# Kernel optimization log

Hardware: AMD Instinct MI355X
Metric: run time of the kernel (lower is better)

## Reference

```python
import jax, jax.numpy as jnp
import numpy as np

H = 512   # hidden_size
V = 128   # vec_size / output_size
L = 8192  # sequence length


def _gru_cell(x, h, Wih, Whh, bih, bhh):
    # torch GRU cell: gates ordered (r, z, n)
    gx = x @ Wih.T + bih            # [3H]
    gh = h @ Whh.T + bhh            # [3H]
    xr, xz, xn = jnp.split(gx, 3)
    hr, hz, hn = jnp.split(gh, 3)
    r = jax.nn.sigmoid(xr + hr)
    z = jax.nn.sigmoid(xz + hz)
    n = jnp.tanh(xn + r * hn)
    return (1.0 - z) * n + z * h


def _run_gru2(xs, h0, h1, p0, p1):
    """2-layer GRU over xs [L, in]; returns ((h0_f, h1_f), top-layer outputs [L, H])."""
    def step(carry, x):
        c0, c1 = carry
        c0 = _gru_cell(x, c0, *p0)
        c1 = _gru_cell(c0, c1, *p1)
        return (c0, c1), c1
    return jax.lax.scan(step, (h0, h1), xs)


def setup_inputs() -> dict:
    key = jax.random.key(0)
    ks = jax.random.split(key, 24)
    b = 1.0 / np.sqrt(H)  # torch default uniform init bound
    u = lambda k, shape: jax.random.uniform(k, shape, jnp.float32, -b, b)
    inp = {
        "src": jax.random.normal(ks[0], (L, V), jnp.float32),
        "trg": jax.random.uniform(ks[1], (L, V), jnp.float32),
        # encoder GRU (input V -> hidden H, 2 layers)
        "enc_Wih0": u(ks[2], (3 * H, V)),  "enc_Whh0": u(ks[3], (3 * H, H)),
        "enc_bih0": u(ks[4], (3 * H,)),    "enc_bhh0": u(ks[5], (3 * H,)),
        "enc_Wih1": u(ks[6], (3 * H, H)),  "enc_Whh1": u(ks[7], (3 * H, H)),
        "enc_bih1": u(ks[8], (3 * H,)),    "enc_bhh1": u(ks[9], (3 * H,)),
        # decoder GRU (input V -> hidden H, 2 layers)
        "dec_Wih0": u(ks[10], (3 * H, V)), "dec_Whh0": u(ks[11], (3 * H, H)),
        "dec_bih0": u(ks[12], (3 * H,)),   "dec_bhh0": u(ks[13], (3 * H,)),
        "dec_Wih1": u(ks[14], (3 * H, H)), "dec_Whh1": u(ks[15], (3 * H, H)),
        "dec_bih1": u(ks[16], (3 * H,)),   "dec_bhh1": u(ks[17], (3 * H,)),
        # output projection
        "Wout": u(ks[18], (V, H)), "bout": u(ks[19], (V,)),
    }
    return inp


def reference(src, trg,
              enc_Wih0, enc_Whh0, enc_bih0, enc_bhh0,
              enc_Wih1, enc_Whh1, enc_bih1, enc_bhh1,
              dec_Wih0, dec_Whh0, dec_bih0, dec_bhh0,
              dec_Wih1, dec_Whh1, dec_bih1, dec_bhh1,
              Wout, bout):
    z = jnp.zeros((H,), src.dtype)
    # Encoder: run 2-layer GRU over src, keep final per-layer states
    (h0, h1), _ = _run_gru2(
        src, z, z,
        (enc_Wih0, enc_Whh0, enc_bih0, enc_bhh0),
        (enc_Wih1, enc_Whh1, enc_bih1, enc_bhh1))
    # Decoder inputs under full teacher forcing: trg[0], trg[0], trg[1], ... trg[L-2]
    dec_in = jax.nn.relu(jnp.concatenate([trg[:1], trg[:-1]], axis=0))  # [L, V]
    _, ys = _run_gru2(
        dec_in, h0, h1,
        (dec_Wih0, dec_Whh0, dec_bih0, dec_bhh0),
        (dec_Wih1, dec_Whh1, dec_bih1, dec_bhh1))  # ys: [L, H] top-layer outputs
    outputs = jax.nn.sigmoid(ys @ Wout.T + bout)   # [L, V]
    return outputs
```

## Files before the change

### kernel.cpp

```cpp
#include <hip/hip_runtime.h>

#define Hh   512
#define Vv   128
#define LL   8192
#define G3   1536
#define NBK  256
#define S0   16
#define S1   4

#define RECBYTES ((S0*512 + S1*512) * 8ull)
#define OFF_GX   0ull
#define OFF_YS   50331648ull
#define OFF_RECE 67108864ull
#define OFF_RECD (OFF_RECE + RECBYTES)
#define OFF_WT   (OFF_RECD + RECBYTES)

#define H1OFF (S0*512)

__device__ __forceinline__ float sigm(float x)  { return 1.f / (1.f + __expf(-x)); }
__device__ __forceinline__ float tanha(float x) { return 2.f / (1.f + __expf(-2.f * x)) - 1.f; }

__device__ __forceinline__ unsigned long long packpair(float v, int t) {
    return ((unsigned long long)(unsigned)t << 32) | (unsigned long long)__float_as_uint(v);
}
__device__ __forceinline__ int   pair_tag(unsigned long long p) { return (int)(p >> 32); }
__device__ __forceinline__ float pair_val(unsigned long long p) { return __uint_as_float((unsigned)p); }

template <int CTRL>
__device__ __forceinline__ float dpp_add(float m) {
    int t = __builtin_amdgcn_update_dpp(0, __builtin_bit_cast(int, m), CTRL, 0xF, 0xF, true);
    return m + __builtin_bit_cast(float, t);
}
__device__ __forceinline__ float red2(float a, float c, int lane) {
    a = dpp_add<0xB1>(a);
    c = dpp_add<0xB1>(c);
    float m = (lane & 1) ? c : a;
    m = dpp_add<0x122>(m);
    m = dpp_add<0x124>(m);
    m = dpp_add<0x128>(m);
    m += __shfl_xor(m, 16);
    m += __shfl_xor(m, 32);
    return m;
}

__global__ __launch_bounds__(256) void gemm_gx(
    const float* __restrict__ X, const float* __restrict__ Wih,
    const float* __restrict__ bih, float* __restrict__ gxo, int shift_relu)
{
    __shared__ float xs[16][128];
    const int tid = threadIdx.x;
    const int m0  = blockIdx.x * 16;
    const int c   = blockIdx.y * 256 + tid;

    for (int i = tid; i < 16 * 128; i += 256) {
        const int r = i >> 7, k = i & 127;
        int srow = m0 + r;
        if (shift_relu) srow = (srow == 0) ? 0 : (srow - 1);
        float v = X[(size_t)srow * Vv + k];
        if (shift_relu) v = fmaxf(v, 0.f);
        xs[r][k] = v;
    }
    __syncthreads();

    const float4* wp = (const float4*)(Wih + (size_t)c * Vv);
    float4 wr[32];
#pragma unroll
    for (int q = 0; q < 32; ++q) wr[q] = wp[q];
    const float bb = bih[c];

    for (int m = 0; m < 16; ++m) {
        const float4* xp = (const float4*)xs[m];
        float acc = bb;
#pragma unroll
        for (int q = 0; q < 32; ++q) {
            const float4 x4 = xp[q];
            acc = fmaf(wr[q].x, x4.x, acc); acc = fmaf(wr[q].y, x4.y, acc);
            acc = fmaf(wr[q].z, x4.z, acc); acc = fmaf(wr[q].w, x4.w, acc);
        }
        gxo[(size_t)(m0 + m) * G3 + c] = acc;
    }
}

__global__ __launch_bounds__(64, 1) void seq2(
    const float* __restrict__ gx,
    const float* __restrict__ Whh0, const float* __restrict__ Wih1,
    const float* __restrict__ Whh1,
    const float* __restrict__ bhh0, const float* __restrict__ bih1,
    const float* __restrict__ bhh1,
    unsigned long long* __restrict__ rec,
    float* __restrict__ ys)
{
    const int bid = blockIdx.x, lane = threadIdx.x;
    unsigned long long* h0rec = rec;
    unsigned long long* h1rec = rec + H1OFF;

    if (bid < 128) {
        const int e0 = 4 * bid;
        int off[8];
#pragma unroll
        for (int j = 0; j < 8; ++j) off[j] = (e0 + lane + 64 * j) & 511;

        float w[12][8];
#pragma unroll
        for (int g = 0; g < 3; ++g)
#pragma unroll
            for (int i = 0; i < 4; ++i) {
                const float* row = Whh0 + (size_t)(g * Hh + e0 + i) * Hh;
#pragma unroll
                for (int j = 0; j < 8; ++j) w[g * 4 + i][j] = row[off[j]];
            }

        float b_r = 0.f, b_z = 0.f, b_n = 0.f;
        if (lane < 4) {
            const int e = e0 + lane;
            b_r = bhh0[e]; b_z = bhh0[Hh + e]; b_n = bhh0[2 * Hh + e];
        }
        float xr = 0.f, xz = 0.f, xn = 0.f;
        if (lane < 4) {
            xr = gx[e0 + lane]; xz = gx[Hh + e0 + lane]; xn = gx[2 * Hh + e0 + lane];
        }

        for (int t = 0; t < LL; ++t) {
            const int need = t - 1;
            const unsigned long long* rp = h0rec + (size_t)((t + S0 - 1) & (S0 - 1)) * 512;
            unsigned long long p[8];
            int ok;
            do {
#pragma unroll
                for (int j = 0; j < 8; ++j)
                    p[j] = __hip_atomic_load(rp + off[j], __ATOMIC_RELAXED, __HIP_MEMORY_SCOPE_AGENT);
                ok = 1;
#pragma unroll
                for (int j = 0; j < 8; ++j) ok &= (pair_tag(p[j]) >= need);
            } while (!__all(ok));

            if ((t & 7) == 0) {
                const int gneed = t - 4;
                const unsigned long long* gp = h1rec + (size_t)(t & (S1 - 1)) * 512;
                int gok;
                do {
                    gok = 1;
#pragma unroll
                    for (int j = 0; j < 8; ++j) {
                        const unsigned long long q = __hip_atomic_load(
                            gp + ((lane + 64 * j) & 511), __ATOMIC_RELAXED, __HIP_MEMORY_SCOPE_AGENT);
                        gok &= (pair_tag(q) >= gneed);
                    }
                } while (!__all(gok));
            }

            float nxr = 0.f, nxz = 0.f, nxn = 0.f;
            if (lane < 4 && t + 1 < LL) {
                const size_t gb = (size_t)(t + 1) * G3 + e0 + lane;
                nxr = gx[gb]; nxz = gx[gb + Hh]; nxn = gx[gb + 2 * Hh];
            }

            float h0v[8];
#pragma unroll
            for (int j = 0; j < 8; ++j) h0v[j] = pair_val(p[j]);

            float acc[12];
#pragma unroll
            for (int r = 0; r < 12; ++r) acc[r] = 0.f;
#pragma unroll
            for (int j = 0; j < 8; ++j)
#pragma unroll
                for (int r = 0; r < 12; ++r) acc[r] = fmaf(w[r][j], h0v[j], acc[r]);

            float sred[6];
#pragma unroll
            for (int k = 0; k < 6; ++k) sred[k] = red2(acc[2 * k], acc[2 * k + 1], lane);

            if (lane < 4) {
                const int i2 = lane >> 1;
                const float rg = sigm(xr + sred[i2] + b_r);
                const float zg = sigm(xz + sred[2 + i2] + b_z);
                const float ng = tanha(xn + rg * (sred[4 + i2] + b_n));
                const float hnew = (1.f - zg) * ng + zg * h0v[0];
                __hip_atomic_store(h0rec + (size_t)(t & (S0 - 1)) * 512 + e0 + lane,
                                   packpair(hnew, t), __ATOMIC_RELAXED, __HIP_MEMORY_SCOPE_AGENT);
            }
            xr = nxr; xz = nxz; xn = nxn;
        }
    } else {
        const int e0 = 4 * (bid - 128);
        int off[8];
#pragma unroll
        for (int j = 0; j < 8; ++j) off[j] = (e0 + lane + 64 * j) & 511;

        float wA[12][8], wB[12][8];
#pragma unroll
        for (int g = 0; g < 3; ++g)
#pragma unroll
            for (int i = 0; i < 4; ++i) {
                const float* rowA = Wih1 + (size_t)(g * Hh + e0 + i) * Hh;
                const float* rowB = Whh1 + (size_t)(g * Hh + e0 + i) * Hh;
#pragma unroll
                for (int j = 0; j < 8; ++j) {
                    wA[g * 4 + i][j] = rowA[off[j]];
                    wB[g * 4 + i][j] = rowB[off[j]];
                }
            }

        float b_r = 0.f, b_z = 0.f, b_n1 = 0.f, b_n2 = 0.f;
        if (lane < 4) {
            const int e = e0 + lane;
            b_r  = bih1[e] + bhh1[e];
            b_z  = bih1[Hh + e] + bhh1[Hh + e];
            b_n1 = bih1[2 * Hh + e];
            b_n2 = bhh1[2 * Hh + e];
        }

        for (int t = 0; t < LL; ++t) {
            const unsigned long long* rp0 = h0rec + (size_t)(t & (S0 - 1)) * 512;
            const unsigned long long* rp1 = h1rec + (size_t)((t + S1 - 1) & (S1 - 1)) * 512;
            unsigned long long p0[8], p1[8];
            int ok;
            do {
#pragma unroll
                for (int j = 0; j < 8; ++j)
                    p0[j] = __hip_atomic_load(rp0 + off[j], __ATOMIC_RELAXED, __HIP_MEMORY_SCOPE_AGENT);
#pragma unroll
                for (int j = 0; j < 8; ++j)
                    p1[j] = __hip_atomic_load(rp1 + off[j], __ATOMIC_RELAXED, __HIP_MEMORY_SCOPE_AGENT);
                ok = 1;
#pragma unroll
                for (int j = 0; j < 8; ++j)
                    ok &= (pair_tag(p0[j]) >= t) & (pair_tag(p1[j]) >= t - 1);
            } while (!__all(ok));

            float h0v[8], h1v[8];
#pragma unroll
            for (int j = 0; j < 8; ++j) { h0v[j] = pair_val(p0[j]); h1v[j] = pair_val(p1[j]); }

            float acc[16];
#pragma unroll
            for (int r = 0; r < 16; ++r) acc[r] = 0.f;
#pragma unroll
            for (int j = 0; j < 8; ++j) {
#pragma unroll
                for (int r = 0; r < 8; ++r) {
                    acc[r] = fmaf(wA[r][j], h0v[j], acc[r]);
                    acc[r] = fmaf(wB[r][j], h1v[j], acc[r]);
                }
#pragma unroll
                for (int i = 0; i < 4; ++i) {
                    acc[8 + i]  = fmaf(wA[8 + i][j], h0v[j], acc[8 + i]);
                    acc[12 + i] = fmaf(wB[8 + i][j], h1v[j], acc[12 + i]);
                }
            }

            float sred[8];
#pragma unroll
            for (int k = 0; k < 8; ++k) sred[k] = red2(acc[2 * k], acc[2 * k + 1], lane);

            if (lane < 4) {
                const int i2 = lane >> 1;
                const float rg = sigm(sred[i2] + b_r);
                const float zg = sigm(sred[2 + i2] + b_z);
                const float ng = tanha(sred[4 + i2] + b_n1 + rg * (sred[6 + i2] + b_n2));
                const float hnew = (1.f - zg) * ng + zg * h1v[0];
                if (ys) ys[(size_t)t * Hh + e0 + lane] = hnew;
                __hip_atomic_store(h1rec + (size_t)(t & (S1 - 1)) * 512 + e0 + lane,
                                   packpair(hnew, t), __ATOMIC_RELAXED, __HIP_MEMORY_SCOPE_AGENT);
            }
        }
    }
}

__global__ __launch_bounds__(256) void transposeW(const float* __restrict__ W,
                                                  float* __restrict__ WT,
                                                  unsigned long long* __restrict__ encr)
{
    const int i = blockIdx.x * 256 + threadIdx.x;
    WT[(i & 511) * 128 + (i >> 9)] = W[i];
    if (i < S0 * 512) {
        const int slot = i >> 9;
        __hip_atomic_store(encr + i, packpair(0.f, (slot == S0 - 1) ? -1 : -100),
                           __ATOMIC_RELAXED, __HIP_MEMORY_SCOPE_AGENT);
    }
    if (i < S1 * 512) {
        const int slot = i >> 9;
        __hip_atomic_store(encr + H1OFF + i, packpair(0.f, (slot == S1 - 1) ? -1 : slot - 4),
                           __ATOMIC_RELAXED, __HIP_MEMORY_SCOPE_AGENT);
    }
}

__global__ __launch_bounds__(256) void handoff(const unsigned long long* __restrict__ encr,
                                               unsigned long long* __restrict__ decr)
{
    const int p = blockIdx.x * 256 + threadIdx.x;
    {
        const int slot = p >> 9;
        unsigned long long v;
        if (slot == S0 - 1) {
            const unsigned long long src = __hip_atomic_load(
                encr + p, __ATOMIC_RELAXED, __HIP_MEMORY_SCOPE_AGENT);
            v = packpair(pair_val(src), -1);
        } else {
            v = packpair(0.f, -100);
        }
        __hip_atomic_store(decr + p, v, __ATOMIC_RELAXED, __HIP_MEMORY_SCOPE_AGENT);
    }
    if (p < S1 * 512) {
        const int slot = p >> 9;
        unsigned long long v;
        if (slot == S1 - 1) {
            const unsigned long long src = __hip_atomic_load(
                encr + H1OFF + p, __ATOMIC_RELAXED, __HIP_MEMORY_SCOPE_AGENT);
            v = packpair(pair_val(src), -1);
        } else {
            v = packpair(0.f, slot - 4);
        }
        __hip_atomic_store(decr + H1OFF + p, v, __ATOMIC_RELAXED, __HIP_MEMORY_SCOPE_AGENT);
    }
}

__global__ __launch_bounds__(128) void out_proj(
    const float* __restrict__ ys, const float* __restrict__ WT,
    const float* __restrict__ bout, float* __restrict__ out)
{
    __shared__ float yss[16][512];
    const int tid = threadIdx.x;
    const int m0  = blockIdx.x * 16;

    for (int i = tid; i < 16 * 512; i += 128)
        yss[i >> 9][i & 511] = ys[(size_t)(m0 + (i >> 9)) * 512 + (i & 511)];
    __syncthreads();

    const int c = tid;
    float acc[16];
    const float b = bout[c];
#pragma unroll
    for (int m = 0; m < 16; ++m) acc[m] = b;

    for (int k4 = 0; k4 < 128; ++k4) {
        const float w0 = WT[(4 * k4 + 0) * 128 + c];
        const float w1 = WT[(4 * k4 + 1) * 128 + c];
        const float w2 = WT[(4 * k4 + 2) * 128 + c];
        const float w3 = WT[(4 * k4 + 3) * 128 + c];
#pragma unroll
        for (int m = 0; m < 16; ++m) {
            const float4 yv = *(const float4*)&yss[m][4 * k4];
            acc[m] = fmaf(w0, yv.x, fmaf(w1, yv.y, fmaf(w2, yv.z, fmaf(w3, yv.w, acc[m]))));
        }
    }
#pragma unroll
    for (int m = 0; m < 16; ++m)
        out[(size_t)(m0 + m) * 128 + c] = 1.f / (1.f + __expf(-acc[m]));
}

extern "C" void kernel_launch(void* const* d_in, const int* in_sizes, int n_in,
                              void* d_out, int out_size, void* d_ws, size_t ws_size,
                              hipStream_t stream)
{
    const float* src      = (const float*)d_in[0];
    const float* trg      = (const float*)d_in[1];
    const float* eWih0    = (const float*)d_in[2];
    const float* eWhh0    = (const float*)d_in[3];
    const float* ebih0    = (const float*)d_in[4];
    const float* ebhh0    = (const float*)d_in[5];
    const float* eWih1    = (const float*)d_in[6];
    const float* eWhh1    = (const float*)d_in[7];
    const float* ebih1    = (const float*)d_in[8];
    const float* ebhh1    = (const float*)d_in[9];
    const float* dWih0    = (const float*)d_in[10];
    const float* dWhh0    = (const float*)d_in[11];
    const float* dbih0    = (const float*)d_in[12];
    const float* dbhh0    = (const float*)d_in[13];
    const float* dWih1    = (const float*)d_in[14];
    const float* dWhh1    = (const float*)d_in[15];
    const float* dbih1    = (const float*)d_in[16];
    const float* dbhh1    = (const float*)d_in[17];
    const float* Wout     = (const float*)d_in[18];
    const float* bout     = (const float*)d_in[19];

    char* ws = (char*)d_ws;
    float*              gx   = (float*)(ws + OFF_GX);
    float*              ys   = (float*)(ws + OFF_YS);
    unsigned long long* recE = (unsigned long long*)(ws + OFF_RECE);
    unsigned long long* recD = (unsigned long long*)(ws + OFF_RECD);
    float*              WT   = (float*)(ws + OFF_WT);

    hipLaunchKernelGGL(transposeW, dim3(256), dim3(256), 0, stream, Wout, WT, recE);

    hipLaunchKernelGGL(gemm_gx, dim3(LL / 16, 6), dim3(256), 0, stream,
                       src, eWih0, ebih0, gx, 0);
    hipLaunchKernelGGL(seq2, dim3(NBK), dim3(64), 0, stream,
                       gx, eWhh0, eWih1, eWhh1, ebhh0, ebih1, ebhh1,
                       recE, (float*)nullptr);

    hipLaunchKernelGGL(handoff, dim3(32), dim3(256), 0, stream, recE, recD);
    hipLaunchKernelGGL(gemm_gx, dim3(LL / 16, 6), dim3(256), 0, stream,
                       trg, dWih0, dbih0, gx, 1);
    hipLaunchKernelGGL(seq2, dim3(NBK), dim3(64), 0, stream,
                       gx, dWhh0, dWih1, dWhh1, dbhh0, dbih1, dbhh1,
                       recD, ys);

    hipLaunchKernelGGL(out_proj, dim3(LL / 16), dim3(128), 0, stream,
                       ys, WT, bout, (float*)d_out);

    (void)in_sizes; (void)n_in; (void)out_size; (void)ws_size;
}
```

Measured before the change: 32.26 ms.

## Consume hidden-state chunks incrementally while spinning and deepen layer-0 ring buffer

```diff
diff --git a/kernel.cpp b/kernel.cpp
--- a/kernel.cpp
+++ b/kernel.cpp
@@ -5,7 +5,7 @@
 #define LL   8192
 #define G3   1536
 #define NBK  256
-#define S0   16
+#define S0   64
 #define S1   4
 
 #define RECBYTES ((S0*512 + S1*512) * 8ull)
@@ -123,19 +123,30 @@
         for (int t = 0; t < LL; ++t) {
             const int need = t - 1;
             const unsigned long long* rp = h0rec + (size_t)((t + S0 - 1) & (S0 - 1)) * 512;
-            unsigned long long p[8];
-            int ok;
+            float acc[12];
+#pragma unroll
+            for (int r = 0; r < 12; ++r) acc[r] = 0.f;
+            float h0self = 0.f;
+            unsigned done = 0;
             do {
+                unsigned long long p[8];
 #pragma unroll
                 for (int j = 0; j < 8; ++j)
                     p[j] = __hip_atomic_load(rp + off[j], __ATOMIC_RELAXED, __HIP_MEMORY_SCOPE_AGENT);
-                ok = 1;
-#pragma unroll
-                for (int j = 0; j < 8; ++j) ok &= (pair_tag(p[j]) >= need);
-            } while (!__all(ok));
-
-            if ((t & 7) == 0) {
-                const int gneed = t - 4;
+#pragma unroll
+                for (int j = 0; j < 8; ++j) {
+                    if (done == (unsigned)j && pair_tag(p[j]) >= need) {
+                        const float v = pair_val(p[j]);
+                        if (j == 0) h0self = v;
+#pragma unroll
+                        for (int r = 0; r < 12; ++r) acc[r] = fmaf(w[r][j], v, acc[r]);
+                        done = j + 1;
+                    }
+                }
+            } while (!__all(done == 8u));
+
+            if ((t & 31) == 0) {
+                const int gneed = t - 16;
                 const unsigned long long* gp = h1rec + (size_t)(t & (S1 - 1)) * 512;
                 int gok;
                 do {
@@ -155,18 +166,6 @@
                 nxr = gx[gb]; nxz = gx[gb + Hh]; nxn = gx[gb + 2 * Hh];
             }
 
-            float h0v[8];
-#pragma unroll
-            for (int j = 0; j < 8; ++j) h0v[j] = pair_val(p[j]);
-
-            float acc[12];
-#pragma unroll
-            for (int r = 0; r < 12; ++r) acc[r] = 0.f;
-#pragma unroll
-            for (int j = 0; j < 8; ++j)
-#pragma unroll
-                for (int r = 0; r < 12; ++r) acc[r] = fmaf(w[r][j], h0v[j], acc[r]);
-
             float sred[6];
 #pragma unroll
             for (int k = 0; k < 6; ++k) sred[k] = red2(acc[2 * k], acc[2 * k + 1], lane);
@@ -176,7 +175,7 @@
                 const float rg = sigm(xr + sred[i2] + b_r);
                 const float zg = sigm(xz + sred[2 + i2] + b_z);
                 const float ng = tanha(xn + rg * (sred[4 + i2] + b_n));
-                const float hnew = (1.f - zg) * ng + zg * h0v[0];
+                const float hnew = (1.f - zg) * ng + zg * h0self;
                 __hip_atomic_store(h0rec + (size_t)(t & (S0 - 1)) * 512 + e0 + lane,
                                    packpair(hnew, t), __ATOMIC_RELAXED, __HIP_MEMORY_SCOPE_AGENT);
             }
@@ -214,52 +213,53 @@
         for (int t = 0; t < LL; ++t) {
             const unsigned long long* rp0 = h0rec + (size_t)(t & (S0 - 1)) * 512;
             const unsigned long long* rp1 = h1rec + (size_t)((t + S1 - 1) & (S1 - 1)) * 512;
-            unsigned long long p0[8], p1[8];
-            int ok;
+            float accA[12], accB[12];
+#pragma unroll
+            for (int r = 0; r < 12; ++r) { accA[r] = 0.f; accB[r] = 0.f; }
+            float h1self = 0.f;
+            unsigned d0 = 0, d1 = 0;
             do {
+                unsigned long long q0[8], q1[8];
 #pragma unroll
                 for (int j = 0; j < 8; ++j)
-                    p0[j] = __hip_atomic_load(rp0 + off[j], __ATOMIC_RELAXED, __HIP_MEMORY_SCOPE_AGENT);
+                    q0[j] = __hip_atomic_load(rp0 + off[j], __ATOMIC_RELAXED, __HIP_MEMORY_SCOPE_AGENT);
 #pragma unroll
                 for (int j = 0; j < 8; ++j)
-                    p1[j] = __hip_atomic_load(rp1 + off[j], __ATOMIC_RELAXED, __HIP_MEMORY_SCOPE_AGENT);
-                ok = 1;
-#pragma unroll
-                for (int j = 0; j < 8; ++j)
-                    ok &= (pair_tag(p0[j]) >= t) & (pair_tag(p1[j]) >= t - 1);
-            } while (!__all(ok));
-
-            float h0v[8], h1v[8];
-#pragma unroll
-            for (int j = 0; j < 8; ++j) { h0v[j] = pair_val(p0[j]); h1v[j] = pair_val(p1[j]); }
-
-            float acc[16];
-#pragma unroll
-            for (int r = 0; r < 16; ++r) acc[r] = 0.f;
-#pragma unroll
-            for (int j = 0; j < 8; ++j) {
-#pragma unroll
-                for (int r = 0; r < 8; ++r) {
-                    acc[r] = fmaf(wA[r][j], h0v[j], acc[r]);
-                    acc[r] = fmaf(wB[r][j], h1v[j], acc[r]);
+                    q1[j] = __hip_atomic_load(rp1 + off[j], __ATOMIC_RELAXED, __HIP_MEMORY_SCOPE_AGENT);
+#pragma unroll
+                for (int j = 0; j < 8; ++j) {
+                    if (d0 == (unsigned)j && pair_tag(q0[j]) >= t) {
+                        const float v = pair_val(q0[j]);
+#pragma unroll
+                        for (int r = 0; r < 12; ++r) accA[r] = fmaf(wA[r][j], v, accA[r]);
+                        d0 = j + 1;
+                    }
+                    if (d1 == (unsigned)j && pair_tag(q1[j]) >= t - 1) {
+                        const float v = pair_val(q1[j]);
+                        if (j == 0) h1self = v;
+#pragma unroll
+                        for (int r = 0; r < 12; ++r) accB[r] = fmaf(wB[r][j], v, accB[r]);
+                        d1 = j + 1;
+                    }
                 }
-#pragma unroll
-                for (int i = 0; i < 4; ++i) {
-                    acc[8 + i]  = fmaf(wA[8 + i][j], h0v[j], acc[8 + i]);
-                    acc[12 + i] = fmaf(wB[8 + i][j], h1v[j], acc[12 + i]);
-                }
-            }
+            } while (!__all((d0 == 8u) & (d1 == 8u)));
 
             float sred[8];
 #pragma unroll
-            for (int k = 0; k < 8; ++k) sred[k] = red2(acc[2 * k], acc[2 * k + 1], lane);
+            for (int k = 0; k < 4; ++k)
+                sred[k] = red2(accA[2 * k] + accB[2 * k], accA[2 * k + 1] + accB[2 * k + 1], lane);
+#pragma unroll
+            for (int k = 0; k < 2; ++k) {
+                sred[4 + k] = red2(accA[8 + 2 * k], accA[9 + 2 * k], lane);
+                sred[6 + k] = red2(accB[8 + 2 * k], accB[9 + 2 * k], lane);
+            }
 
             if (lane < 4) {
                 const int i2 = lane >> 1;
                 const float rg = sigm(sred[i2] + b_r);
                 const float zg = sigm(sred[2 + i2] + b_z);
                 const float ng = tanha(sred[4 + i2] + b_n1 + rg * (sred[6 + i2] + b_n2));
-                const float hnew = (1.f - zg) * ng + zg * h1v[0];
+                const float hnew = (1.f - zg) * ng + zg * h1self;
                 if (ys) ys[(size_t)t * Hh + e0 + lane] = hnew;
                 __hip_atomic_store(h1rec + (size_t)(t & (S1 - 1)) * 512 + e0 + lane,
                                    packpair(hnew, t), __ATOMIC_RELAXED, __HIP_MEMORY_SCOPE_AGENT);
@@ -390,7 +390,7 @@
                        gx, eWhh0, eWih1, eWhh1, ebhh0, ebih1, ebhh1,
                        recE, (float*)nullptr);
 
-    hipLaunchKernelGGL(handoff, dim3(32), dim3(256), 0, stream, recE, recD);
+    hipLaunchKernelGGL(handoff, dim3(128), dim3(256), 0, stream, recE, recD);
     hipLaunchKernelGGL(gemm_gx, dim3(LL / 16, 6), dim3(256), 0, stream,
                        trg, dWih0, dbih0, gx, 1);
     hipLaunchKernelGGL(seq2, dim3(NBK), dim3(64), 0, stream,
```

Result: slower. 49.44 ms (+53.3%).

## Prefetch next-step hidden state speculatively and widen layer-0 ring buffer

Applied to the files above, without the earlier changes.

```diff
diff --git a/kernel.cpp b/kernel.cpp
--- a/kernel.cpp
+++ b/kernel.cpp
@@ -5,7 +5,7 @@
 #define LL   8192
 #define G3   1536
 #define NBK  256
-#define S0   16
+#define S0   64
 #define S1   4
 
 #define RECBYTES ((S0*512 + S1*512) * 8ull)
@@ -25,6 +25,9 @@
 }
 __device__ __forceinline__ int   pair_tag(unsigned long long p) { return (int)(p >> 32); }
 __device__ __forceinline__ float pair_val(unsigned long long p) { return __uint_as_float((unsigned)p); }
+
+#define ALOAD(p) __hip_atomic_load((p), __ATOMIC_RELAXED, __HIP_MEMORY_SCOPE_AGENT)
+#define ASTORE(p, v) __hip_atomic_store((p), (v), __ATOMIC_RELAXED, __HIP_MEMORY_SCOPE_AGENT)
 
 template <int CTRL>
 __device__ __forceinline__ float dpp_add(float m) {
@@ -120,30 +123,42 @@
             xr = gx[e0 + lane]; xz = gx[Hh + e0 + lane]; xn = gx[2 * Hh + e0 + lane];
         }
 
+        unsigned long long ownpk = ALOAD(h0rec + (size_t)(S0 - 1) * 512 + e0 + (lane & 3));
+        unsigned long long pr[8];
+        {
+            const unsigned long long* rp0 = h0rec + (size_t)(S0 - 1) * 512;
+#pragma unroll
+            for (int j = 0; j < 8; ++j) pr[j] = ALOAD(rp0 + off[j]);
+        }
+
         for (int t = 0; t < LL; ++t) {
             const int need = t - 1;
             const unsigned long long* rp = h0rec + (size_t)((t + S0 - 1) & (S0 - 1)) * 512;
             unsigned long long p[8];
-            int ok;
-            do {
-#pragma unroll
-                for (int j = 0; j < 8; ++j)
-                    p[j] = __hip_atomic_load(rp + off[j], __ATOMIC_RELAXED, __HIP_MEMORY_SCOPE_AGENT);
+#pragma unroll
+            for (int j = 0; j < 8; ++j) p[j] = pr[j];
+            if (lane < 4) p[0] = ownpk;
+            int ok = 1;
+#pragma unroll
+            for (int j = 0; j < 8; ++j) ok &= (pair_tag(p[j]) >= need);
+            while (!__all(ok)) {
+#pragma unroll
+                for (int j = 0; j < 8; ++j) p[j] = ALOAD(rp + off[j]);
+                if (lane < 4) p[0] = ownpk;
                 ok = 1;
 #pragma unroll
                 for (int j = 0; j < 8; ++j) ok &= (pair_tag(p[j]) >= need);
-            } while (!__all(ok));
-
-            if ((t & 7) == 0) {
-                const int gneed = t - 4;
+            }
+
+            if ((t & 31) == 0) {
+                const int gneed = t - 16;
                 const unsigned long long* gp = h1rec + (size_t)(t & (S1 - 1)) * 512;
                 int gok;
                 do {
                     gok = 1;
 #pragma unroll
                     for (int j = 0; j < 8; ++j) {
-                        const unsigned long long q = __hip_atomic_load(
-                            gp + ((lane + 64 * j) & 511), __ATOMIC_RELAXED, __HIP_MEMORY_SCOPE_AGENT);
+                        const unsigned long long q = ALOAD(gp + ((lane + 64 * j) & 511));
                         gok &= (pair_tag(q) >= gneed);
                     }
                 } while (!__all(gok));
@@ -177,8 +192,14 @@
                 const float zg = sigm(xz + sred[2 + i2] + b_z);
                 const float ng = tanha(xn + rg * (sred[4 + i2] + b_n));
                 const float hnew = (1.f - zg) * ng + zg * h0v[0];
-                __hip_atomic_store(h0rec + (size_t)(t & (S0 - 1)) * 512 + e0 + lane,
-                                   packpair(hnew, t), __ATOMIC_RELAXED, __HIP_MEMORY_SCOPE_AGENT);
+                ownpk = packpair(hnew, t);
+                ASTORE(h0rec + (size_t)(t & (S0 - 1)) * 512 + e0 + lane, ownpk);
+            }
+
+            {
+                const unsigned long long* rpn = h0rec + (size_t)(t & (S0 - 1)) * 512;
+#pragma unroll
+                for (int j = 0; j < 8; ++j) pr[j] = ALOAD(rpn + off[j]);
             }
             xr = nxr; xz = nxz; xn = nxn;
         }
@@ -211,23 +232,39 @@
             b_n2 = bhh1[2 * Hh + e];
         }
 
+        unsigned long long ownpk1 = ALOAD(h1rec + (size_t)(S1 - 1) * 512 + e0 + (lane & 3));
+        unsigned long long pr0[8], pr1[8];
+        {
+            const unsigned long long* a = h0rec;
+            const unsigned long long* b = h1rec + (size_t)(S1 - 1) * 512;
+#pragma unroll
+            for (int j = 0; j < 8; ++j) pr0[j] = ALOAD(a + off[j]);
+#pragma unroll
+            for (int j = 0; j < 8; ++j) pr1[j] = ALOAD(b + off[j]);
+        }
+
         for (int t = 0; t < LL; ++t) {
             const unsigned long long* rp0 = h0rec + (size_t)(t & (S0 - 1)) * 512;
             const unsigned long long* rp1 = h1rec + (size_t)((t + S1 - 1) & (S1 - 1)) * 512;
             unsigned long long p0[8], p1[8];
-            int ok;
-            do {
-#pragma unroll
-                for (int j = 0; j < 8; ++j)
-                    p0[j] = __hip_atomic_load(rp0 + off[j], __ATOMIC_RELAXED, __HIP_MEMORY_SCOPE_AGENT);
-#pragma unroll
-                for (int j = 0; j < 8; ++j)
-                    p1[j] = __hip_atomic_load(rp1 + off[j], __ATOMIC_RELAXED, __HIP_MEMORY_SCOPE_AGENT);
+#pragma unroll
+            for (int j = 0; j < 8; ++j) { p0[j] = pr0[j]; p1[j] = pr1[j]; }
+            if (lane < 4) p1[0] = ownpk1;
+            int ok = 1;
+#pragma unroll
+            for (int j = 0; j < 8; ++j)
+                ok &= (pair_tag(p0[j]) >= t) & (pair_tag(p1[j]) >= t - 1);
+            while (!__all(ok)) {
+#pragma unroll
+                for (int j = 0; j < 8; ++j) p0[j] = ALOAD(rp0 + off[j]);
+#pragma unroll
+                for (int j = 0; j < 8; ++j) p1[j] = ALOAD(rp1 + off[j]);
+                if (lane < 4) p1[0] = ownpk1;
                 ok = 1;
 #pragma unroll
                 for (int j = 0; j < 8; ++j)
                     ok &= (pair_tag(p0[j]) >= t) & (pair_tag(p1[j]) >= t - 1);
-            } while (!__all(ok));
+            }
 
             float h0v[8], h1v[8];
 #pragma unroll
@@ -260,9 +297,18 @@
                 const float zg = sigm(sred[2 + i2] + b_z);
                 const float ng = tanha(sred[4 + i2] + b_n1 + rg * (sred[6 + i2] + b_n2));
                 const float hnew = (1.f - zg) * ng + zg * h1v[0];
+                ownpk1 = packpair(hnew, t);
+                ASTORE(h1rec + (size_t)(t & (S1 - 1)) * 512 + e0 + lane, ownpk1);
                 if (ys) ys[(size_t)t * Hh + e0 + lane] = hnew;
-                __hip_atomic_store(h1rec + (size_t)(t & (S1 - 1)) * 512 + e0 + lane,
-                                   packpair(hnew, t), __ATOMIC_RELAXED, __HIP_MEMORY_SCOPE_AGENT);
+            }
+
+            {
+                const unsigned long long* a = h0rec + (size_t)((t + 1) & (S0 - 1)) * 512;
+                const unsigned long long* b = h1rec + (size_t)(t & (S1 - 1)) * 512;
+#pragma unroll
+                for (int j = 0; j < 8; ++j) pr0[j] = ALOAD(a + off[j]);
+#pragma unroll
+                for (int j = 0; j < 8; ++j) pr1[j] = ALOAD(b + off[j]);
             }
         }
     }
@@ -276,13 +322,11 @@
     WT[(i & 511) * 128 + (i >> 9)] = W[i];
     if (i < S0 * 512) {
         const int slot = i >> 9;
-        __hip_atomic_store(encr + i, packpair(0.f, (slot == S0 - 1) ? -1 : -100),
-                           __ATOMIC_RELAXED, __HIP_MEMORY_SCOPE_AGENT);
+        ASTORE(encr + i, packpair(0.f, (slot == S0 - 1) ? -1 : -100));
     }
     if (i < S1 * 512) {
         const int slot = i >> 9;
-        __hip_atomic_store(encr + H1OFF + i, packpair(0.f, (slot == S1 - 1) ? -1 : slot - 4),
-                           __ATOMIC_RELAXED, __HIP_MEMORY_SCOPE_AGENT);
+        ASTORE(encr + H1OFF + i, packpair(0.f, (slot == S1 - 1) ? -1 : slot - 4));
     }
 }
 
@@ -294,25 +338,23 @@
         const int slot = p >> 9;
         unsigned long long v;
         if (slot == S0 - 1) {
-            const unsigned long long src = __hip_atomic_load(
-                encr + p, __ATOMIC_RELAXED, __HIP_MEMORY_SCOPE_AGENT);
+            const unsigned long long src = ALOAD(encr + p);
             v = packpair(pair_val(src), -1);
         } else {
             v = packpair(0.f, -100);
         }
-        __hip_atomic_store(decr + p, v, __ATOMIC_RELAXED, __HIP_MEMORY_SCOPE_AGENT);
+        ASTORE(decr + p, v);
     }
     if (p < S1 * 512) {
         const int slot = p >> 9;
         unsigned long long v;
         if (slot == S1 - 1) {
-            const unsigned long long src = __hip_atomic_load(
-                encr + H1OFF + p, __ATOMIC_RELAXED, __HIP_MEMORY_SCOPE_AGENT);
+            const unsigned long long src = ALOAD(encr + H1OFF + p);
             v = packpair(pair_val(src), -1);
         } else {
             v = packpair(0.f, slot - 4);
         }
-        __hip_atomic_store(decr + H1OFF + p, v, __ATOMIC_RELAXED, __HIP_MEMORY_SCOPE_AGENT);
+        ASTORE(decr + H1OFF + p, v);
     }
 }
 
@@ -390,7 +432,7 @@
                        gx, eWhh0, eWih1, eWhh1, ebhh0, ebih1, ebhh1,
                        recE, (float*)nullptr);
 
-    hipLaunchKernelGGL(handoff, dim3(32), dim3(256), 0, stream, recE, recD);
+    hipLaunchKernelGGL(handoff, dim3(128), dim3(256), 0, stream, recE, recD);
     hipLaunchKernelGGL(gemm_gx, dim3(LL / 16, 6), dim3(256), 0, stream,
                        trg, dWih0, dbih0, gx, 1);
     hipLaunchKernelGGL(seq2, dim3(NBK), dim3(64), 0, stream,
```

Measured after the change: 35.01 ms. +8.5%, slower.
